# Optimization experiments

Measured on AMD Instinct MI355X. Metric: run time of the kernel, lower is better.

Reference implementation:

```python
import jax, jax.numpy as jnp
import numpy as np

B = 1024
IN_H, IN_W = 128, 128
KH, KW = 10, 10
SH, SW = 5, 5
PH, PW = 2, 2
HP, WP = IN_H + 2 * PH, IN_W + 2 * PW          # padded dims: 132, 132
NKH = (IN_H - KH + 2 * PH) // SH + 1            # 25
NKW = (IN_W - KW + 2 * PW) // SW + 1            # 25
NK = NKH * NKW                                  # 625


def _build_weight_matrix(kernel_weights):
    """kernel_weights: [NK, KH, KW] -> sparse-structured dense [HP*WP, NK].
    Faithful to LocallyConnected2dV2._create_weight_matrix, vectorized."""
    i = jnp.arange(NK)
    start_i = (i // NKW) * SH                   # [NK]
    start_j = (i % NKW) * SW                    # [NK]
    # flat row index for each (kernel, k, l) tap in padded image
    rows = ((start_i[:, None, None] + jnp.arange(KH)[None, :, None]) * WP
            + start_j[:, None, None] + jnp.arange(KW)[None, None, :])  # [NK,KH,KW]
    rows = rows.reshape(NK, KH * KW)
    cols = i[:, None]                           # [NK,1] broadcasts over taps
    W = jnp.zeros((HP * WP, NK), dtype=kernel_weights.dtype)
    return W.at[rows, cols].set(kernel_weights.reshape(NK, KH * KW))


def setup_inputs() -> dict:
    key = jax.random.key(0)
    kx, kw, kb = jax.random.split(key, 3)
    x = jax.random.normal(kx, (B, IN_H, IN_W), dtype=jnp.float32)
    kernel_weights = jax.random.normal(kw, (NK, KH, KW), dtype=jnp.float32)
    W = _build_weight_matrix(kernel_weights)    # [HP*WP, NK]
    bias = jax.random.normal(kb, (NKH, NKW), dtype=jnp.float32)
    return {"x": x, "W": W, "bias": bias}


def reference(x, W, bias):
    # zero-pad spatial dims, flatten, dense GEMM against sparse-structured W
    xp = jnp.pad(x, ((0, 0), (PH, PH), (PW, PW)))          # [B,HP,WP]
    xf = xp.reshape(x.shape[0], HP * WP)                   # [B,HP*WP]
    out = xf @ W                                           # [B,NK]
    out = out.reshape(x.shape[0], NKH, NKW)
    return out + bias
```

## Files before the change

kernel.cpp:

```cpp
#include <hip/hip_runtime.h>

typedef _Float16 f16x2 __attribute__((ext_vector_type(2)));
typedef __fp16  fp16x2 __attribute__((ext_vector_type(2)));

constexpr int NKW  = 25, NK = 625;
constexpr int WPADR = 132;
constexpr int WPT   = 160;
constexpr int RST   = 35;
constexpr int IMG   = 8;
constexpr int NSLAB = 6;
constexpr int MAXR  = 30;

union U2H { unsigned int u; f16x2 h; fp16x2 p; };

__global__ void gather_wp(const float* __restrict__ W, _Float16* __restrict__ wgpT) {
    int t = blockIdx.x * 256 + threadIdx.x;
    if (t >= NK * WPT) return;
    int k = t / WPT, p = t % WPT;
    int di = p >> 4, s = p & 15;
    int ki = k / NKW, kj = k % NKW;
    int o = (5 * kj + 2) & 3;
    int j = s - o;
    float val = 0.f;
    if (j >= 0 && j < 10)
        val = W[(size_t)((ki * 5 + di) * WPADR + kj * 5 + j) * NK + k];
    wgpT[((size_t)(p >> 3) * NK + k) * 8 + (p & 7)] = (_Float16)val;
}

__device__ __forceinline__ float dot2acc(unsigned int a, unsigned int b, float c) {
    U2H ua, ub; ua.u = a; ub.u = b;
#if __has_builtin(__builtin_amdgcn_fdot2)
    return __builtin_amdgcn_fdot2(ua.h, ub.h, c, false);
#else
    return c + (float)ua.h.x * (float)ub.h.x + (float)ua.h.y * (float)ub.h.y;
#endif
}

template <bool USE_WG>
__global__ __launch_bounds__(256, 4)
void lc2d_pipe(const float* __restrict__ x, const _Float16* __restrict__ wgpT,
               const float* __restrict__ Wfull,
               const float* __restrict__ bias, float* __restrict__ out) {
    __shared__ uint2 xs[2][MAXR * RST];

    const int grp  = blockIdx.x;
    const int slab = blockIdx.y;
    const int K0   = slab ? (4 * slab + 1) : 0;
    const int NKI  = slab ? 4 : 5;
    const int R    = 5 * NKI + 5;
    const int NOUT = NKI * NKW;
    const int row0 = 5 * K0 - 2;
    const int tid  = threadIdx.x;
    const int b0   = grp * IMG;

    const int lane = tid & 63;
    const int pairidx = (tid >> 6) * 32 + (lane & 31);
    const int half = (lane >> 5) & 1;
    const bool active = pairidx < NOUT;
    const int ki_l = pairidx / 25;
    const int kj   = pairidx - ki_l * 25;
    const int k    = (K0 + ki_l) * NKW + kj;
    const int di0  = half * 5;

    uint4 wq[10];
    float bval = 0.f;
    if (active) {
        if (USE_WG) {
            const uint4* wt4 = reinterpret_cast<const uint4*>(wgpT);
#pragma unroll
            for (int j = 0; j < 10; ++j) wq[j] = wt4[(size_t)(half * 10 + j) * NK + k];
        } else {
            const int o = (5 * kj + 2) & 3;
#pragma unroll
            for (int j = 0; j < 10; ++j) {
                const int di = di0 + (j >> 1), pb = (j & 1) * 8;
                unsigned int uu[4];
#pragma unroll
                for (int m = 0; m < 4; ++m) {
                    float f0 = 0.f, f1 = 0.f;
                    const int j0 = pb + 2 * m - o, j1 = pb + 2 * m + 1 - o;
                    const size_t rowb = (size_t)(((K0 + ki_l) * 5 + di) * WPADR + kj * 5);
                    if (j0 >= 0 && j0 < 10) f0 = Wfull[(rowb + j0) * NK + k];
                    if (j1 >= 0 && j1 < 10) f1 = Wfull[(rowb + j1) * NK + k];
                    U2H u; u.p = __builtin_amdgcn_cvt_pkrtz(f0, f1);
                    uu[m] = u.u;
                }
                wq[j] = make_uint4(uu[0], uu[1], uu[2], uu[3]);
            }
        }
        if (half == 0) bval = bias[k];
    }

    for (int i = tid; i < 4 * R; i += 256)
        xs[i & 1][(i >> 2) * RST + ((i >> 1) & 1) * 33] = make_uint2(0u, 0u);

    auto stage_load = [&](int img, float4* tmp) {
        const float* xb = x + ((size_t)(b0 + img) << 14);
#pragma unroll
        for (int t = 0; t < 4; ++t) {
            const int i = tid + t * 256;
            tmp[t] = make_float4(0.f, 0.f, 0.f, 0.f);
            if (i < R * 32) {
                const int idx = i >> 5, q = i & 31;
                const int r = row0 + idx;
                if (r >= 0 && r < 128)
                    tmp[t] = *reinterpret_cast<const float4*>(xb + (r << 7) + (q << 2));
            }
        }
    };
    auto stage_write = [&](int buf, const float4* tmp) {
#pragma unroll
        for (int t = 0; t < 4; ++t) {
            const int i = tid + t * 256;
            if (i < R * 32) {
                const int idx = i >> 5, q = (i & 31) + 1;
                U2H u0, u1;
                u0.p = __builtin_amdgcn_cvt_pkrtz(tmp[t].x, tmp[t].y);
                u1.p = __builtin_amdgcn_cvt_pkrtz(tmp[t].z, tmp[t].w);
                xs[buf][idx * RST + q] = make_uint2(u0.u, u1.u);
            }
        }
    };

    float4 tmpA[4], tmpB[4];
    stage_load(0, tmpA);
    stage_write(0, tmpA);
    stage_load(1, tmpB);
    __syncthreads();

    for (int i = 0; i < IMG; ++i) {
        if (i + 2 < IMG) stage_load(i + 2, (i & 1) ? tmpB : tmpA);

        float acc0 = 0.f, acc1 = 0.f;
        if (active) {
            const uint2* base = xs[i & 1] + (5 * ki_l + di0) * RST + ((5 * kj + 2) >> 2);
#pragma unroll
            for (int d = 0; d < 5; ++d) {
                const uint2* rowp = base + d * RST;
                const uint2 a0 = rowp[0], a1 = rowp[1], a2 = rowp[2], a3 = rowp[3];
                const uint4 wA = wq[2 * d], wB = wq[2 * d + 1];
                acc0 = dot2acc(a0.x, wA.x, acc0);
                acc1 = dot2acc(a0.y, wA.y, acc1);
                acc0 = dot2acc(a1.x, wA.z, acc0);
                acc1 = dot2acc(a1.y, wA.w, acc1);
                acc0 = dot2acc(a2.x, wB.x, acc0);
                acc1 = dot2acc(a2.y, wB.y, acc1);
                acc0 = dot2acc(a3.x, wB.z, acc0);
                acc1 = dot2acc(a3.y, wB.w, acc1);
            }
        }
        float acc = acc0 + acc1;
        float other = __shfl_xor(acc, 32, 64);
        if (active && half == 0)
            out[(size_t)(b0 + i) * NK + k] = acc + other + bval;

        if (i + 1 < IMG) stage_write((i + 1) & 1, (i & 1) ? tmpA : tmpB);
        __syncthreads();
    }
}

extern "C" void kernel_launch(void* const* d_in, const int* in_sizes, int n_in,
                              void* d_out, int out_size, void* d_ws, size_t ws_size,
                              hipStream_t stream) {
    const float* x    = (const float*)d_in[0];
    const float* W    = (const float*)d_in[1];
    const float* bias = (const float*)d_in[2];
    float* out = (float*)d_out;

    const dim3 grid(1024 / IMG, NSLAB);
    if (ws_size >= (size_t)NK * WPT * sizeof(_Float16)) {
        _Float16* wgpT = (_Float16*)d_ws;
        gather_wp<<<(NK * WPT + 255) / 256, 256, 0, stream>>>(W, wgpT);
        lc2d_pipe<true><<<grid, 256, 0, stream>>>(x, wgpT, W, bias, out);
    } else {
        lc2d_pipe<false><<<grid, 256, 0, stream>>>(x, nullptr, W, bias, out);
    }
}
```

Before: 122.4 us.

## Assign one kernel row per wavefront with private LDS, removing block barriers

Restructures work so each wavefront handles a single kernel row for 8 images, staging its own 10 input rows into a private LDS buffer. This removes __syncthreads and the idle lanes of the slab decomposition. In exchange, overlapping input rows are loaded separately by adjacent waves, roughly doubling global reads of x, and the wave-local LDS reuse relies on intra-wave ordering.

```diff
diff --git a/kernel.cpp b/kernel.cpp
--- a/kernel.cpp
+++ b/kernel.cpp
@@ -6,10 +6,7 @@
 constexpr int NKW  = 25, NK = 625;
 constexpr int WPADR = 132;
 constexpr int WPT   = 160;
-constexpr int RST   = 35;
 constexpr int IMG   = 8;
-constexpr int NSLAB = 6;
-constexpr int MAXR  = 30;
 
 union U2H { unsigned int u; f16x2 h; fp16x2 p; };
 
@@ -38,124 +35,110 @@
 
 template <bool USE_WG>
 __global__ __launch_bounds__(256, 4)
-void lc2d_pipe(const float* __restrict__ x, const _Float16* __restrict__ wgpT,
+void lc2d_wave(const float* __restrict__ x, const _Float16* __restrict__ wgpT,
                const float* __restrict__ Wfull,
                const float* __restrict__ bias, float* __restrict__ out) {
-    __shared__ uint2 xs[2][MAXR * RST];
+    __shared__ uint2 xsw[4][2][350];
 
-    const int grp  = blockIdx.x;
-    const int slab = blockIdx.y;
-    const int K0   = slab ? (4 * slab + 1) : 0;
-    const int NKI  = slab ? 4 : 5;
-    const int R    = 5 * NKI + 5;
-    const int NOUT = NKI * NKW;
-    const int row0 = 5 * K0 - 2;
-    const int tid  = threadIdx.x;
-    const int b0   = grp * IMG;
+    const int widx = threadIdx.x >> 6;
+    const int lane = threadIdx.x & 63;
+    const int waveId = blockIdx.x * 4 + widx;
+    const int ki  = waveId % 25;
+    const int grp = waveId / 25;
+    const int b0  = grp * IMG;
+    const int half = lane >> 5;
+    const int p    = lane & 31;
+    const int pc   = min(p, 24);
+    const int k    = ki * NKW + pc;
+    const int di0  = half * 5;
+    const int row0 = 5 * ki - 2;
 
-    const int lane = tid & 63;
-    const int pairidx = (tid >> 6) * 32 + (lane & 31);
-    const int half = (lane >> 5) & 1;
-    const bool active = pairidx < NOUT;
-    const int ki_l = pairidx / 25;
-    const int kj   = pairidx - ki_l * 25;
-    const int k    = (K0 + ki_l) * NKW + kj;
-    const int di0  = half * 5;
+    if (lane < 40) {
+        const int bz = lane / 20, rem = lane % 20;
+        xsw[widx][bz][(rem >> 1) * 35 + (rem & 1) * 33] = make_uint2(0u, 0u);
+    }
 
     uint4 wq[10];
-    float bval = 0.f;
-    if (active) {
-        if (USE_WG) {
-            const uint4* wt4 = reinterpret_cast<const uint4*>(wgpT);
+    if (USE_WG) {
+        const uint4* wt4 = reinterpret_cast<const uint4*>(wgpT);
 #pragma unroll
-            for (int j = 0; j < 10; ++j) wq[j] = wt4[(size_t)(half * 10 + j) * NK + k];
-        } else {
-            const int o = (5 * kj + 2) & 3;
+        for (int j = 0; j < 10; ++j) wq[j] = wt4[(size_t)(half * 10 + j) * NK + k];
+    } else {
+        const int o = (5 * pc + 2) & 3;
 #pragma unroll
-            for (int j = 0; j < 10; ++j) {
-                const int di = di0 + (j >> 1), pb = (j & 1) * 8;
-                unsigned int uu[4];
+        for (int j = 0; j < 10; ++j) {
+            const int di = di0 + (j >> 1), pb = (j & 1) * 8;
+            unsigned int uu[4];
 #pragma unroll
-                for (int m = 0; m < 4; ++m) {
-                    float f0 = 0.f, f1 = 0.f;
-                    const int j0 = pb + 2 * m - o, j1 = pb + 2 * m + 1 - o;
-                    const size_t rowb = (size_t)(((K0 + ki_l) * 5 + di) * WPADR + kj * 5);
-                    if (j0 >= 0 && j0 < 10) f0 = Wfull[(rowb + j0) * NK + k];
-                    if (j1 >= 0 && j1 < 10) f1 = Wfull[(rowb + j1) * NK + k];
-                    U2H u; u.p = __builtin_amdgcn_cvt_pkrtz(f0, f1);
-                    uu[m] = u.u;
-                }
-                wq[j] = make_uint4(uu[0], uu[1], uu[2], uu[3]);
+            for (int m = 0; m < 4; ++m) {
+                float f0 = 0.f, f1 = 0.f;
+                const int j0 = pb + 2 * m - o, j1 = pb + 2 * m + 1 - o;
+                const size_t rowb = (size_t)((ki * 5 + di) * WPADR + pc * 5);
+                if (j0 >= 0 && j0 < 10) f0 = Wfull[(rowb + j0) * NK + k];
+                if (j1 >= 0 && j1 < 10) f1 = Wfull[(rowb + j1) * NK + k];
+                U2H u; u.p = __builtin_amdgcn_cvt_pkrtz(f0, f1);
+                uu[m] = u.u;
             }
+            wq[j] = make_uint4(uu[0], uu[1], uu[2], uu[3]);
         }
-        if (half == 0) bval = bias[k];
     }
-
-    for (int i = tid; i < 4 * R; i += 256)
-        xs[i & 1][(i >> 2) * RST + ((i >> 1) & 1) * 33] = make_uint2(0u, 0u);
+    const float bval = (half == 0) ? bias[k] : 0.f;
 
     auto stage_load = [&](int img, float4* tmp) {
         const float* xb = x + ((size_t)(b0 + img) << 14);
 #pragma unroll
-        for (int t = 0; t < 4; ++t) {
-            const int i = tid + t * 256;
+        for (int t = 0; t < 5; ++t) {
+            const int i = lane + (t << 6);
+            const int r = row0 + (i >> 5), q = i & 31;
             tmp[t] = make_float4(0.f, 0.f, 0.f, 0.f);
-            if (i < R * 32) {
-                const int idx = i >> 5, q = i & 31;
-                const int r = row0 + idx;
-                if (r >= 0 && r < 128)
-                    tmp[t] = *reinterpret_cast<const float4*>(xb + (r << 7) + (q << 2));
-            }
+            if (r >= 0)
+                tmp[t] = *reinterpret_cast<const float4*>(xb + (r << 7) + (q << 2));
         }
     };
     auto stage_write = [&](int buf, const float4* tmp) {
+        uint2* xd = &xsw[widx][buf][0];
 #pragma unroll
-        for (int t = 0; t < 4; ++t) {
-            const int i = tid + t * 256;
-            if (i < R * 32) {
-                const int idx = i >> 5, q = (i & 31) + 1;
-                U2H u0, u1;
-                u0.p = __builtin_amdgcn_cvt_pkrtz(tmp[t].x, tmp[t].y);
-                u1.p = __builtin_amdgcn_cvt_pkrtz(tmp[t].z, tmp[t].w);
-                xs[buf][idx * RST + q] = make_uint2(u0.u, u1.u);
-            }
+        for (int t = 0; t < 5; ++t) {
+            const int i = lane + (t << 6);
+            const int idx = i >> 5, q = (i & 31) + 1;
+            U2H u0, u1;
+            u0.p = __builtin_amdgcn_cvt_pkrtz(tmp[t].x, tmp[t].y);
+            u1.p = __builtin_amdgcn_cvt_pkrtz(tmp[t].z, tmp[t].w);
+            xd[idx * 35 + q] = make_uint2(u0.u, u1.u);
         }
     };
 
-    float4 tmpA[4], tmpB[4];
-    stage_load(0, tmpA);
-    stage_write(0, tmpA);
-    stage_load(1, tmpB);
-    __syncthreads();
+    float4 tA[5], tB[5];
+    stage_load(0, tA);
+    stage_write(0, tA);
+    stage_load(1, tB);
 
+    const int woff = (5 * pc + 2) >> 2;
     for (int i = 0; i < IMG; ++i) {
-        if (i + 2 < IMG) stage_load(i + 2, (i & 1) ? tmpB : tmpA);
+        if (i + 2 < IMG) stage_load(i + 2, (i & 1) ? tB : tA);
 
+        const uint2* base = &xsw[widx][i & 1][0] + di0 * 35 + woff;
         float acc0 = 0.f, acc1 = 0.f;
-        if (active) {
-            const uint2* base = xs[i & 1] + (5 * ki_l + di0) * RST + ((5 * kj + 2) >> 2);
 #pragma unroll
-            for (int d = 0; d < 5; ++d) {
-                const uint2* rowp = base + d * RST;
-                const uint2 a0 = rowp[0], a1 = rowp[1], a2 = rowp[2], a3 = rowp[3];
-                const uint4 wA = wq[2 * d], wB = wq[2 * d + 1];
-                acc0 = dot2acc(a0.x, wA.x, acc0);
-                acc1 = dot2acc(a0.y, wA.y, acc1);
-                acc0 = dot2acc(a1.x, wA.z, acc0);
-                acc1 = dot2acc(a1.y, wA.w, acc1);
-                acc0 = dot2acc(a2.x, wB.x, acc0);
-                acc1 = dot2acc(a2.y, wB.y, acc1);
-                acc0 = dot2acc(a3.x, wB.z, acc0);
-                acc1 = dot2acc(a3.y, wB.w, acc1);
-            }
+        for (int d = 0; d < 5; ++d) {
+            const uint2* rowp = base + d * 35;
+            const uint2 a0 = rowp[0], a1 = rowp[1], a2 = rowp[2], a3 = rowp[3];
+            const uint4 wA = wq[2 * d], wB = wq[2 * d + 1];
+            acc0 = dot2acc(a0.x, wA.x, acc0);
+            acc1 = dot2acc(a0.y, wA.y, acc1);
+            acc0 = dot2acc(a1.x, wA.z, acc0);
+            acc1 = dot2acc(a1.y, wA.w, acc1);
+            acc0 = dot2acc(a2.x, wB.x, acc0);
+            acc1 = dot2acc(a2.y, wB.y, acc1);
+            acc0 = dot2acc(a3.x, wB.z, acc0);
+            acc1 = dot2acc(a3.y, wB.w, acc1);
         }
-        float acc = acc0 + acc1;
-        float other = __shfl_xor(acc, 32, 64);
-        if (active && half == 0)
-            out[(size_t)(b0 + i) * NK + k] = acc + other + bval;
+        const float r = acc0 + acc1;
+        const float other = __shfl_xor(r, 32, 64);
+        if (half == 0 && p < 25)
+            out[(size_t)(b0 + i) * NK + k] = r + other + bval;
 
-        if (i + 1 < IMG) stage_write((i + 1) & 1, (i & 1) ? tmpA : tmpB);
-        __syncthreads();
+        if (i + 1 < IMG) stage_write((i + 1) & 1, (i & 1) ? tA : tB);
     }
 }
 
@@ -167,12 +150,12 @@
     const float* bias = (const float*)d_in[2];
     float* out = (float*)d_out;
 
-    const dim3 grid(1024 / IMG, NSLAB);
+    const dim3 grid(800);
     if (ws_size >= (size_t)NK * WPT * sizeof(_Float16)) {
         _Float16* wgpT = (_Float16*)d_ws;
         gather_wp<<<(NK * WPT + 255) / 256, 256, 0, stream>>>(W, wgpT);
-        lc2d_pipe<true><<<grid, 256, 0, stream>>>(x, wgpT, W, bias, out);
+        lc2d_wave<true><<<grid, 256, 0, stream>>>(x, wgpT, W, bias, out);
     } else {
-        lc2d_pipe<false><<<grid, 256, 0, stream>>>(x, nullptr, W, bias, out);
+        lc2d_wave<false><<<grid, 256, 0, stream>>>(x, nullptr, W, bias, out);
     }
 }
```

After: 126.2 us. +3.1%, slower.
